# Performance work log

Hardware: AMD Instinct MI355X
Metric: run time of the kernel (lower is better)

## Reference

```python
import jax, jax.numpy as jnp
import numpy as np

LATENT = 128   # latent_size
FDIM = 32      # feature_dim per plane
FSIZE = 512    # feature_size -> grid is (FSIZE+1)^2
HID = 256      # hidden_dim
N = 500000     # number of query points
IN_DIM = 3
G = FSIZE + 1
SDF_IN = 3 * FDIM + LATENT + IN_DIM  # 227


def setup_inputs() -> dict:
    key = jax.random.key(0)
    ks = jax.random.split(key, 6)
    x = jax.random.normal(ks[0], (N, LATENT + IN_DIM), jnp.float32)
    # 3 tri-planes, each [FDIM, G, G], init randn*0.01 as in FeaturePlanes
    P = jax.random.normal(ks[1], (3, FDIM, G, G), jnp.float32) * 0.01

    def lin(k, fan_in, fan_out):
        s = 1.0 / np.sqrt(fan_in)
        kw, kb = jax.random.split(k)
        W = jax.random.uniform(kw, (fan_in, fan_out), jnp.float32, -s, s)
        b = jax.random.uniform(kb, (fan_out,), jnp.float32, -s, s)
        return W, b

    W0, b0 = lin(ks[2], SDF_IN, HID)
    W1, b1 = lin(ks[3], HID, HID)
    W2, b2 = lin(ks[4], HID, 1)
    return dict(x=x, P=P, W0=W0, b0=b0, W1=W1, b1=b1, W2=W2, b2=b2)


def _sample_plane(plane, uv):
    """Bilinear grid_sample, align_corners=True, padding_mode='border'.
    plane: [C, G, G]; uv: [Npts, 2] with uv[:,0]->width(x), uv[:,1]->height(y).
    Returns [Npts, C]."""
    g = jnp.clip((uv + 1.0) * 0.5 * (G - 1), 0.0, G - 1)  # unnormalize + border clamp
    gx, gy = g[:, 0], g[:, 1]
    x0f, y0f = jnp.floor(gx), jnp.floor(gy)
    x0 = x0f.astype(jnp.int32)
    y0 = y0f.astype(jnp.int32)
    x1 = jnp.minimum(x0 + 1, G - 1)
    y1 = jnp.minimum(y0 + 1, G - 1)
    wx = gx - x0f
    wy = gy - y0f
    v00 = plane[:, y0, x0]  # [C, Npts]
    v01 = plane[:, y0, x1]
    v10 = plane[:, y1, x0]
    v11 = plane[:, y1, x1]
    top = v00 * (1.0 - wx) + v01 * wx
    bot = v10 * (1.0 - wx) + v11 * wx
    return (top * (1.0 - wy) + bot * wy).T  # [Npts, C]


def reference(x, P, W0, b0, W1, b1, W2, b2):
    in_latents = x[:, :LATENT]
    in_x = x[:, -3:]
    coords = jax.lax.stop_gradient(in_x)  # matches .detach() before grid_sample
    # dimension pairs (0,1), (0,2), (1,2) -> one bilinear lookup each, vmapped
    uv = jnp.stack([coords[:, [0, 1]], coords[:, [0, 2]], coords[:, [1, 2]]])  # [3,N,2]
    feats = jax.vmap(_sample_plane)(P, uv)              # [3, N, FDIM]
    feats = jnp.transpose(feats, (1, 0, 2)).reshape(x.shape[0], 3 * FDIM)
    net_in = jnp.concatenate([in_latents, in_x, feats], axis=-1)  # [N, 227]
    h = jax.nn.relu(net_in @ W0 + b0)
    h = jax.nn.relu(h @ W1 + b1)
    out = (h @ W2 + b2).squeeze(-1)  # [N]
    return out
```

## Files before the change

### kernel.cpp

```cpp
#include <hip/hip_runtime.h>
#include <stdint.h>

#define XDIM 131
#define LATENT 128
#define FDIM 32
#define GSZ 513
#define HID 256
#define SDF_IN 227

typedef __attribute__((ext_vector_type(8))) short bf16x8;
typedef __attribute__((ext_vector_type(4))) float f32x4;
typedef unsigned short ushort_t;
typedef unsigned int uint32;

__device__ __forceinline__ unsigned short f2bf(float f) {
  uint32 u = __float_as_uint(f);
  u += 0x7fffu + ((u >> 16) & 1u);
  return (unsigned short)(u >> 16);
}
__device__ __forceinline__ float bf2f(unsigned short s) {
  return __uint_as_float(((uint32)s) << 16);
}

__global__ void prep_pt(const float* __restrict__ P, unsigned short* __restrict__ Pt) {
  int i = blockIdx.x * 256 + threadIdx.x;
  const int CELLS = 3 * GSZ * GSZ;
  if (i >= CELLS) return;
  int pl = i / (GSZ * GSZ);
  int yx = i - pl * (GSZ * GSZ);
  const float* src = P + (size_t)pl * FDIM * GSZ * GSZ + yx;
  union { unsigned short u[32]; uint4 v[4]; } t;
#pragma unroll
  for (int c = 0; c < 32; ++c)
    t.u[c] = f2bf(src[(size_t)c * (GSZ * GSZ)]);
  uint4* dst = (uint4*)(Pt + (size_t)i * 32);
#pragma unroll
  for (int w = 0; w < 4; ++w) dst[w] = t.v[w];
}

__global__ void prep_w(const float* __restrict__ W0, const float* __restrict__ W1,
                       unsigned short* __restrict__ W0g, unsigned short* __restrict__ W1g) {
  int i = blockIdx.x * 256 + threadIdx.x;
  int sel = i >> 13;
  int t = i & 8191;
  int ks = t >> 10;
  int g  = (t >> 8) & 3;
  int n  = t & 255;
  union { unsigned short u[8]; uint4 v; } o;
#pragma unroll
  for (int j = 0; j < 8; ++j) {
    int k = ks * 32 + g * 8 + j;
    float val;
    if (sel == 0) val = (k < SDF_IN) ? W0[k * 256 + n] : 0.f;
    else          val = W1[k * 256 + n];
    o.u[j] = f2bf(val);
  }
  unsigned short* dst = (sel == 0 ? W0g : W1g) + (size_t)t * 8;
  *(uint4*)dst = o.v;
}

__device__ __forceinline__ int act_addr(int r, int c) {
  return ((c >> 5) * 4 + ((c >> 3) & 3)) * 1024 + r * 8 + (c & 7);
}

__device__ __forceinline__ void gemm_layer(unsigned short* act,
                                           const unsigned short* __restrict__ Wg,
                                           const float* __restrict__ bias,
                                           int rg, int cg, int lr, int lg)
{
  f32x4 acc[4][4];
#pragma unroll
  for (int mf = 0; mf < 4; ++mf)
#pragma unroll
    for (int nf = 0; nf < 4; ++nf) acc[mf][nf] = (f32x4){0.f, 0.f, 0.f, 0.f};

  float bs[4];
#pragma unroll
  for (int nf = 0; nf < 4; ++nf) bs[nf] = bias[cg * 64 + nf * 16 + lr];

#pragma unroll
  for (int kb = 0; kb < 8; ++kb) {
    bf16x8 a[4], b[4];
#pragma unroll
    for (int mf = 0; mf < 4; ++mf)
      a[mf] = *(const bf16x8*)(act + kb * 4096 + lg * 1024 + (rg * 64 + mf * 16 + lr) * 8);
#pragma unroll
    for (int nf = 0; nf < 4; ++nf)
      b[nf] = *(const bf16x8*)(Wg + (size_t)(kb * 4 + lg) * 2048 + (cg * 64 + nf * 16 + lr) * 8);
#pragma unroll
    for (int mf = 0; mf < 4; ++mf)
#pragma unroll
      for (int nf = 0; nf < 4; ++nf)
        acc[mf][nf] = __builtin_amdgcn_mfma_f32_16x16x32_bf16(a[mf], b[nf], acc[mf][nf], 0, 0, 0);
  }
  __syncthreads();
#pragma unroll
  for (int mf = 0; mf < 4; ++mf)
#pragma unroll
    for (int nf = 0; nf < 4; ++nf) {
      int c = cg * 64 + nf * 16 + lr;
      unsigned short* dst = act + ((c >> 5) * 4 + ((c >> 3) & 3)) * 1024 + (c & 7);
#pragma unroll
      for (int reg = 0; reg < 4; ++reg) {
        int r = rg * 64 + mf * 16 + lg * 4 + reg;
        float vv = fmaxf(acc[mf][nf][reg] + bs[nf], 0.f);
        dst[r * 8] = f2bf(vv);
      }
    }
  __syncthreads();
}

template<int USE_PT>
__global__ __launch_bounds__(512) void sdf_main(
    const float* __restrict__ x, const float* __restrict__ P,
    const unsigned short* __restrict__ Pt,
    const unsigned short* __restrict__ W0g, const unsigned short* __restrict__ W1g,
    const float* __restrict__ b0, const float* __restrict__ b1,
    const float* __restrict__ W2, const float* __restrict__ b2v,
    float* __restrict__ out, int Npts)
{
  __shared__ unsigned short act[128 * 256];

  const int tid = threadIdx.x;
  const int p0 = blockIdx.x * 128;

  {
    uint4 z = {0u, 0u, 0u, 0u};
    uint4* zb = (uint4*)(act + 7 * 4096);
    if (tid < 512) zb[tid] = z;
  }
  __syncthreads();

  for (int idx = tid; idx < 128 * XDIM; idx += 512) {
    int r = idx / XDIM;
    int c = idx - r * XDIM;
    int p = p0 + r; if (p >= Npts) p = Npts - 1;
    float v = x[(size_t)p * XDIM + c];
    act[act_addr(r, c)] = f2bf(v);
  }

  {
    int p_l = tid >> 2;
    int q = tid & 3;
    int p = p0 + p_l; if (p >= Npts) p = Npts - 1;
    float cc0 = x[(size_t)p * XDIM + LATENT + 0];
    float cc1 = x[(size_t)p * XDIM + LATENT + 1];
    float cc2 = x[(size_t)p * XDIM + LATENT + 2];
#pragma unroll
    for (int pl = 0; pl < 3; ++pl) {
      float u = (pl == 2) ? cc1 : cc0;
      float v = (pl == 0) ? cc1 : cc2;
      float gx = fminf(fmaxf((u + 1.f) * 256.f, 0.f), 512.f);
      float gy = fminf(fmaxf((v + 1.f) * 256.f, 0.f), 512.f);
      float x0f = floorf(gx), y0f = floorf(gy);
      int x0 = (int)x0f, y0 = (int)y0f;
      int x1 = min(x0 + 1, GSZ - 1), y1 = min(y0 + 1, GSZ - 1);
      float wx = gx - x0f, wy = gy - y0f;
      float w00 = (1.f - wx) * (1.f - wy), w01 = wx * (1.f - wy);
      float w10 = (1.f - wx) * wy,        w11 = wx * wy;
      float f[8];
      if (USE_PT) {
        const uint4 v00 = *(const uint4*)(Pt + ((size_t)((pl * GSZ + y0) * GSZ + x0)) * 32 + q * 8);
        const uint4 v01 = *(const uint4*)(Pt + ((size_t)((pl * GSZ + y0) * GSZ + x1)) * 32 + q * 8);
        const uint4 v10 = *(const uint4*)(Pt + ((size_t)((pl * GSZ + y1) * GSZ + x0)) * 32 + q * 8);
        const uint4 v11 = *(const uint4*)(Pt + ((size_t)((pl * GSZ + y1) * GSZ + x1)) * 32 + q * 8);
#pragma unroll
        for (int j = 0; j < 8; ++j) {
          f[j] = w00 * bf2f(((const unsigned short*)&v00)[j])
               + w01 * bf2f(((const unsigned short*)&v01)[j])
               + w10 * bf2f(((const unsigned short*)&v10)[j])
               + w11 * bf2f(((const unsigned short*)&v11)[j]);
        }
      } else {
#pragma unroll
        for (int j = 0; j < 8; ++j) {
          int c = q * 8 + j;
          const float* pc = P + (size_t)(pl * FDIM + c) * GSZ * GSZ;
          f[j] = w00 * pc[y0 * GSZ + x0] + w01 * pc[y0 * GSZ + x1]
               + w10 * pc[y1 * GSZ + x0] + w11 * pc[y1 * GSZ + x1];
        }
      }
#pragma unroll
      for (int j = 0; j < 8; ++j) {
        int c = XDIM + pl * FDIM + q * 8 + j;
        act[act_addr(p_l, c)] = f2bf(f[j]);
      }
    }
  }
  __syncthreads();

  const int lane = tid & 63, wid = tid >> 6;
  const int rg = wid >> 2, cg = wid & 3, lr = lane & 15, lg = lane >> 4;

  gemm_layer(act, W0g, b0, rg, cg, lr, lg);
  gemm_layer(act, W1g, b1, rg, cg, lr, lg);

  {
    int p_l = tid >> 2, q = tid & 3;
    float sum = 0.f;
#pragma unroll
    for (int j = 0; j < 64; ++j) {
      int c = q * 64 + j;
      sum += bf2f(act[act_addr(p_l, c)]) * W2[c];
    }
    sum += __shfl_xor(sum, 1);
    sum += __shfl_xor(sum, 2);
    if (q == 0) {
      int p = p0 + p_l;
      if (p < Npts) out[p] = sum + b2v[0];
    }
  }
}

extern "C" void kernel_launch(void* const* d_in, const int* in_sizes, int n_in,
                              void* d_out, int out_size, void* d_ws, size_t ws_size,
                              hipStream_t stream)
{
  const float* x  = (const float*)d_in[0];
  const float* P  = (const float*)d_in[1];
  const float* W0 = (const float*)d_in[2];
  const float* b0 = (const float*)d_in[3];
  const float* W1 = (const float*)d_in[4];
  const float* b1 = (const float*)d_in[5];
  const float* W2 = (const float*)d_in[6];
  const float* b2 = (const float*)d_in[7];
  float* out = (float*)d_out;
  int Npts = in_sizes[0] / XDIM;

  const size_t PT_BYTES = (size_t)3 * GSZ * GSZ * 32 * 2;
  const size_t WG_BYTES = (size_t)8192 * 8 * 2;
  char* ws = (char*)d_ws;
  int use_pt = (ws_size >= PT_BYTES + 2 * WG_BYTES) ? 1 : 0;
  unsigned short *Ptb, *W0g, *W1g;
  if (use_pt) {
    Ptb = (unsigned short*)ws;
    W0g = (unsigned short*)(ws + PT_BYTES);
    W1g = (unsigned short*)(ws + PT_BYTES + WG_BYTES);
  } else {
    Ptb = nullptr;
    W0g = (unsigned short*)ws;
    W1g = (unsigned short*)(ws + WG_BYTES);
  }

  prep_w<<<64, 256, 0, stream>>>(W0, W1, W0g, W1g);
  if (use_pt) prep_pt<<<(3 * GSZ * GSZ + 255) / 256, 256, 0, stream>>>(P, Ptb);

  int nblk = (Npts + 127) / 128;
  if (use_pt)
    sdf_main<1><<<nblk, 512, 0, stream>>>(x, P, Ptb, W0g, W1g, b0, b1, W2, b2, out, Npts);
  else
    sdf_main<0><<<nblk, 512, 0, stream>>>(x, P, Ptb, W0g, W1g, b0, b1, W2, b2, out, Npts);
}
```

Measured before the change: 304.9 us.

## Pad and swizzle LDS activation layout, align feature columns, vectorize staging

Reworks the shared-memory activation layout with a padded block stride and an XOR swizzle on row slots to cut LDS bank conflicts. Feature columns are moved to start at an 8-aligned offset (136), and W0 is remapped to match, so sampled features and x rows can be written as 16-byte vector stores instead of scalar stores. The final dot product with W2 now uses vector LDS and global loads, and launch bounds request 4 blocks per CU. The remapped W0 padding and zeroed gap blocks must stay consistent with the new column layout, or results will be wrong.

```diff
diff --git a/kernel.cpp b/kernel.cpp
--- a/kernel.cpp
+++ b/kernel.cpp
@@ -5,12 +5,12 @@
 #define LATENT 128
 #define FDIM 32
 #define GSZ 513
-#define HID 256
 #define SDF_IN 227
+#define FEAT0 136
+#define BSTRIDE 2064
 
 typedef __attribute__((ext_vector_type(8))) short bf16x8;
 typedef __attribute__((ext_vector_type(4))) float f32x4;
-typedef unsigned short ushort_t;
 typedef unsigned int uint32;
 
 __device__ __forceinline__ unsigned short f2bf(float f) {
@@ -20,6 +20,12 @@
 }
 __device__ __forceinline__ float bf2f(unsigned short s) {
   return __uint_as_float(((uint32)s) << 16);
+}
+
+__device__ __forceinline__ int slot16(int r) { return (r * 16) ^ (((r >> 3) & 1) << 5); }
+__device__ __forceinline__ int blk_of(int c) { return (c >> 5) * 4 + ((c >> 3) & 3); }
+__device__ __forceinline__ int act_byte(int r, int c) {
+  return blk_of(c) * BSTRIDE + slot16(r) + (c & 7) * 2;
 }
 
 __global__ void prep_pt(const float* __restrict__ P, unsigned short* __restrict__ Pt) {
@@ -43,27 +49,27 @@
   int i = blockIdx.x * 256 + threadIdx.x;
   int sel = i >> 13;
   int t = i & 8191;
-  int ks = t >> 10;
+  int kb = t >> 10;
   int g  = (t >> 8) & 3;
   int n  = t & 255;
   union { unsigned short u[8]; uint4 v; } o;
 #pragma unroll
   for (int j = 0; j < 8; ++j) {
-    int k = ks * 32 + g * 8 + j;
+    int k = kb * 32 + g * 8 + j;
     float val;
-    if (sel == 0) val = (k < SDF_IN) ? W0[k * 256 + n] : 0.f;
-    else          val = W1[k * 256 + n];
+    if (sel == 0) {
+      int src = (k < 131) ? k : ((k >= FEAT0 && k < FEAT0 + 96) ? k - 5 : -1);
+      val = (src >= 0) ? W0[src * 256 + n] : 0.f;
+    } else {
+      val = W1[k * 256 + n];
+    }
     o.u[j] = f2bf(val);
   }
   unsigned short* dst = (sel == 0 ? W0g : W1g) + (size_t)t * 8;
   *(uint4*)dst = o.v;
 }
 
-__device__ __forceinline__ int act_addr(int r, int c) {
-  return ((c >> 5) * 4 + ((c >> 3) & 3)) * 1024 + r * 8 + (c & 7);
-}
-
-__device__ __forceinline__ void gemm_layer(unsigned short* act,
+__device__ __forceinline__ void gemm_layer(unsigned char* actb,
                                            const unsigned short* __restrict__ Wg,
                                            const float* __restrict__ bias,
                                            int rg, int cg, int lr, int lg)
@@ -81,12 +87,13 @@
 #pragma unroll
   for (int kb = 0; kb < 8; ++kb) {
     bf16x8 a[4], b[4];
+    const int ab = (kb * 4 + lg) * BSTRIDE;
 #pragma unroll
     for (int mf = 0; mf < 4; ++mf)
-      a[mf] = *(const bf16x8*)(act + kb * 4096 + lg * 1024 + (rg * 64 + mf * 16 + lr) * 8);
+      a[mf] = *(const bf16x8*)(actb + ab + slot16(rg * 64 + mf * 16 + lr));
 #pragma unroll
     for (int nf = 0; nf < 4; ++nf)
-      b[nf] = *(const bf16x8*)(Wg + (size_t)(kb * 4 + lg) * 2048 + (cg * 64 + nf * 16 + lr) * 8);
+      b[nf] = *(const bf16x8*)(Wg + (size_t)(kb * 4 + lg) * 2048 + (size_t)(cg * 64 + nf * 16 + lr) * 8);
 #pragma unroll
     for (int mf = 0; mf < 4; ++mf)
 #pragma unroll
@@ -99,19 +106,19 @@
 #pragma unroll
     for (int nf = 0; nf < 4; ++nf) {
       int c = cg * 64 + nf * 16 + lr;
-      unsigned short* dst = act + ((c >> 5) * 4 + ((c >> 3) & 3)) * 1024 + (c & 7);
+      unsigned char* dst = actb + blk_of(c) * BSTRIDE + (c & 7) * 2;
 #pragma unroll
       for (int reg = 0; reg < 4; ++reg) {
         int r = rg * 64 + mf * 16 + lg * 4 + reg;
         float vv = fmaxf(acc[mf][nf][reg] + bs[nf], 0.f);
-        dst[r * 8] = f2bf(vv);
+        *(unsigned short*)(dst + slot16(r)) = f2bf(vv);
       }
     }
   __syncthreads();
 }
 
 template<int USE_PT>
-__global__ __launch_bounds__(512) void sdf_main(
+__global__ __launch_bounds__(512, 4) void sdf_main(
     const float* __restrict__ x, const float* __restrict__ P,
     const unsigned short* __restrict__ Pt,
     const unsigned short* __restrict__ W0g, const unsigned short* __restrict__ W1g,
@@ -119,33 +126,43 @@
     const float* __restrict__ W2, const float* __restrict__ b2v,
     float* __restrict__ out, int Npts)
 {
-  __shared__ unsigned short act[128 * 256];
+  __shared__ __align__(16) unsigned char actb[32 * BSTRIDE];
 
   const int tid = threadIdx.x;
   const int p0 = blockIdx.x * 128;
 
   {
     uint4 z = {0u, 0u, 0u, 0u};
-    uint4* zb = (uint4*)(act + 7 * 4096);
-    if (tid < 512) zb[tid] = z;
-  }
-  __syncthreads();
-
-  for (int idx = tid; idx < 128 * XDIM; idx += 512) {
-    int r = idx / XDIM;
-    int c = idx - r * XDIM;
-    int p = p0 + r; if (p >= Npts) p = Npts - 1;
-    float v = x[(size_t)p * XDIM + c];
-    act[act_addr(r, c)] = f2bf(v);
+    if (tid < 129)      ((uint4*)(actb + 16 * BSTRIDE))[tid] = z;
+    else if (tid < 516) ((uint4*)(actb + 29 * BSTRIDE))[tid - 129] = z;
+  }
+  __syncthreads();
+
+#pragma unroll
+  for (int i = 0; i < 4; ++i) {
+    int t = i * 512 + tid;
+    int cb = t & 15, r = t >> 4;
+    int p = min(p0 + r, Npts - 1);
+    const float* src = x + (size_t)p * XDIM + cb * 8;
+    union { unsigned short u[8]; uint4 v; } h;
+#pragma unroll
+    for (int j = 0; j < 8; ++j) h.u[j] = f2bf(src[j]);
+    *(uint4*)(actb + cb * BSTRIDE + slot16(r)) = h.v;
+  }
+  if (tid < 128) {
+    int r = tid;
+    int p = min(p0 + r, Npts - 1);
+#pragma unroll
+    for (int j = 0; j < 3; ++j)
+      *(unsigned short*)(actb + act_byte(r, 128 + j)) = f2bf(x[(size_t)p * XDIM + 128 + j]);
   }
 
   {
     int p_l = tid >> 2;
     int q = tid & 3;
-    int p = p0 + p_l; if (p >= Npts) p = Npts - 1;
-    float cc0 = x[(size_t)p * XDIM + LATENT + 0];
-    float cc1 = x[(size_t)p * XDIM + LATENT + 1];
-    float cc2 = x[(size_t)p * XDIM + LATENT + 2];
+    int p = min(p0 + p_l, Npts - 1);
+    const float* xr = x + (size_t)p * XDIM + LATENT;
+    float cc0 = xr[0], cc1 = xr[1], cc2 = xr[2];
 #pragma unroll
     for (int pl = 0; pl < 3; ++pl) {
       float u = (pl == 2) ? cc1 : cc0;
@@ -180,11 +197,10 @@
                + w10 * pc[y1 * GSZ + x0] + w11 * pc[y1 * GSZ + x1];
         }
       }
-#pragma unroll
-      for (int j = 0; j < 8; ++j) {
-        int c = XDIM + pl * FDIM + q * 8 + j;
-        act[act_addr(p_l, c)] = f2bf(f[j]);
-      }
+      union { unsigned short u16[8]; uint4 v4; } fo;
+#pragma unroll
+      for (int j = 0; j < 8; ++j) fo.u16[j] = f2bf(f[j]);
+      *(uint4*)(actb + (17 + pl * 4 + q) * BSTRIDE + slot16(p_l)) = fo.v4;
     }
   }
   __syncthreads();
@@ -192,16 +208,22 @@
   const int lane = tid & 63, wid = tid >> 6;
   const int rg = wid >> 2, cg = wid & 3, lr = lane & 15, lg = lane >> 4;
 
-  gemm_layer(act, W0g, b0, rg, cg, lr, lg);
-  gemm_layer(act, W1g, b1, rg, cg, lr, lg);
+  gemm_layer(actb, W0g, b0, rg, cg, lr, lg);
+  gemm_layer(actb, W1g, b1, rg, cg, lr, lg);
 
   {
     int p_l = tid >> 2, q = tid & 3;
     float sum = 0.f;
 #pragma unroll
-    for (int j = 0; j < 64; ++j) {
-      int c = q * 64 + j;
-      sum += bf2f(act[act_addr(p_l, c)]) * W2[c];
+    for (int m = 0; m < 8; ++m) {
+      int cbase = m * 32 + q * 8;
+      bf16x8 h = *(const bf16x8*)(actb + (m * 4 + q) * BSTRIDE + slot16(p_l));
+      float4 wa = *(const float4*)(W2 + cbase);
+      float4 wb = *(const float4*)(W2 + cbase + 4);
+      sum += bf2f((unsigned short)h[0]) * wa.x + bf2f((unsigned short)h[1]) * wa.y
+           + bf2f((unsigned short)h[2]) * wa.z + bf2f((unsigned short)h[3]) * wa.w
+           + bf2f((unsigned short)h[4]) * wb.x + bf2f((unsigned short)h[5]) * wb.y
+           + bf2f((unsigned short)h[6]) * wb.z + bf2f((unsigned short)h[7]) * wb.w;
     }
     sum += __shfl_xor(sum, 1);
     sum += __shfl_xor(sum, 2);
```

Measured after the change: 340.8 us. 1.12x slower.
